# Kernel optimization log

Measured on AMD Instinct MI355X. Metric: run time of the kernel, lower is better.

The kernel has to match this reference:

```python
import jax, jax.numpy as jnp
import numpy as np

B, N, D = 1, 4096, 512
H, DH, M, WIN = 8, 64, 4, 512
QK_SCALE = 10.0  # qk_norm_scale


def _l2norm(t):
    # F.normalize(p=2, dim=-1) with groups=1
    n = jnp.linalg.norm(t, axis=-1, keepdims=True)
    return t / jnp.maximum(n, 1e-12)


def _rotate_half(t):
    t1, t2 = jnp.split(t, 2, axis=-1)
    return jnp.concatenate([-t2, t1], axis=-1)


def setup_inputs() -> dict:
    key = jax.random.key(0)
    ks = jax.random.split(key, 9)
    s = 0.02
    x = jax.random.normal(ks[0], (B, N, D), jnp.float32)
    Wq = jax.random.normal(ks[1], (D, H * DH), jnp.float32) * s
    Wk = jax.random.normal(ks[2], (D, H * DH), jnp.float32) * s
    Wv = jax.random.normal(ks[3], (D, H * DH), jnp.float32) * s
    Wg = jax.random.normal(ks[4], (D, H * DH), jnp.float32) * s
    bg = jnp.ones((H * DH,), jnp.float32)  # torch init: bias=1
    Wo = jax.random.normal(ks[5], (H * DH, D), jnp.float32) * s
    mem_k = jax.random.normal(ks[6], (H, M, DH), jnp.float32)
    mem_v = jax.random.normal(ks[7], (H, M, DH), jnp.float32)
    # standard rotary table, duplicated halves so rotate_half pairing matches
    half = DH // 2
    inv = 1.0 / (10000.0 ** (np.arange(half, dtype=np.float32) / half))
    f = np.outer(np.arange(N, dtype=np.float32), inv)  # [N, DH/2]
    freqs = jnp.asarray(np.concatenate([f, f], axis=-1), jnp.float32)  # [N, DH]
    return {"x": x, "Wq": Wq, "Wk": Wk, "Wv": Wv, "Wg": Wg, "bg": bg,
            "Wo": Wo, "mem_k": mem_k, "mem_v": mem_v, "freqs": freqs}


def reference(x, Wq, Wk, Wv, Wg, bg, Wo, mem_k, mem_v, freqs):
    # projections -> b h n d
    def split_heads(t):
        return t.reshape(B, N, H, DH).transpose(0, 2, 1, 3)
    q = split_heads(x @ Wq)
    k = split_heads(x @ Wk)
    v = split_heads(x @ Wv)
    # qk-norm (groups=1), scale handled via QK_SCALE later
    q = _l2norm(q)
    k = _l2norm(k)
    # rotary (l == DH so full head dim is rotated)
    cos = jnp.cos(freqs)  # [N, DH]
    sin = jnp.sin(freqs)
    q = q * cos + _rotate_half(q) * sin
    k = k * cos + _rotate_half(k) * sin
    # memory KV concat (mem_k goes through l2norm under qk_norm)
    mk = jnp.broadcast_to(_l2norm(mem_k)[None], (B, H, M, DH))
    mv = jnp.broadcast_to(mem_v[None], (B, H, M, DH))
    k = jnp.concatenate([mk, k], axis=2)  # [B,H,M+N,DH]
    v = jnp.concatenate([mv, v], axis=2)
    J = N + M
    # local window mask: queries at positions M..J-1, keys at 0..J-1
    rq = jnp.arange(M, J)
    rk = jnp.arange(J)
    dist = rq[:, None] - rk[None, :]
    allowed = (dist <= WIN) & (dist >= -WIN)  # [N, J]
    sim = jnp.einsum('bhid,bhjd->bhij', q, k) * QK_SCALE
    neg = -jnp.finfo(sim.dtype).max
    sim = jnp.where(allowed[None, None], sim, neg)
    attn = jax.nn.softmax(sim, axis=-1)
    out = jnp.einsum('bhij,bhjd->bhid', attn, v)  # [B,H,N,DH]
    out = out.transpose(0, 2, 1, 3).reshape(B, N, H * DH)
    # value gating
    gates = x @ Wg + bg
    out = out * jax.nn.sigmoid(gates)
    return out @ Wo
```

## Files before the change

### kernel.cpp

```cpp
#include <hip/hip_runtime.h>
#include <math.h>

#define TN 4096
#define DM 512
#define NH 8
#define DHD 64
#define MEM 4
#define WINR 512
#define JTOT (TN + MEM)
#define JPAD 4168
#define QK_SCALE 10.0f

typedef __attribute__((ext_vector_type(8))) short bf16x8;
typedef __attribute__((ext_vector_type(4))) float f32x4;

__device__ __forceinline__ unsigned short f2bf(float f) {
    unsigned u = __float_as_uint(f);
    u = (u + 0x7FFFu + ((u >> 16) & 1u)) >> 16;
    return (unsigned short)u;
}

__global__ __launch_bounds__(256)
void prep(const float* __restrict__ X, unsigned short* __restrict__ Xb,
          const float* __restrict__ W0, const float* __restrict__ W1,
          const float* __restrict__ W2, const float* __restrict__ W3,
          const float* __restrict__ W4, unsigned short* __restrict__ T,
          const float* __restrict__ freqs, float2* __restrict__ tab,
          const float* __restrict__ mem_k, const float* __restrict__ mem_v,
          unsigned short* __restrict__ k_b, unsigned short* __restrict__ v_b)
{
    const int b = blockIdx.x;
    const int t = threadIdx.x;

    if (b < 2048) {
        int idx = b * 256 + t;
        float4 v = *(const float4*)&X[(size_t)idx * 4];
        *(ushort4*)&Xb[(size_t)idx * 4] =
            make_ushort4(f2bf(v.x), f2bf(v.y), f2bf(v.z), f2bf(v.w));
    } else if (b < 2368) {
        __shared__ unsigned short Ts[64][68];
        int bi = b - 2048;
        int sel = bi >> 6, tile = bi & 63;
        const float* __restrict__ W =
            (sel == 0) ? W0 : (sel == 1) ? W1 : (sel == 2) ? W2 : (sel == 3) ? W3 : W4;
        unsigned short* __restrict__ Wt = T + (size_t)sel * DM * DM;
        int r0 = (tile >> 3) * 64, c0 = (tile & 7) * 64;
        #pragma unroll
        for (int p = 0; p < 4; ++p) {
            int i  = p * 16 + (t >> 4);
            int j4 = (t & 15) * 4;
            float4 v = *(const float4*)&W[(size_t)(r0 + i) * DM + c0 + j4];
            Ts[i][j4 + 0] = f2bf(v.x); Ts[i][j4 + 1] = f2bf(v.y);
            Ts[i][j4 + 2] = f2bf(v.z); Ts[i][j4 + 3] = f2bf(v.w);
        }
        __syncthreads();
        #pragma unroll
        for (int p = 0; p < 4; ++p) {
            int oc  = p * 16 + (t >> 4);
            int or4 = (t & 15) * 4;
            *(ushort4*)&Wt[(size_t)(c0 + oc) * DM + r0 + or4] =
                make_ushort4(Ts[or4 + 0][oc], Ts[or4 + 1][oc],
                             Ts[or4 + 2][oc], Ts[or4 + 3][oc]);
        }
    } else if (b < 2432) {
        int tid = (b - 2368) * 256 + t;
        #pragma unroll
        for (int e = 0; e < 16; ++e) {
            int id = e * 16384 + tid;
            float f = freqs[id];
            float sn, cs;
            sincosf(f, &sn, &cs);
            tab[id] = make_float2(cs, sn);
        }
    } else {
        int gw   = (b - 2432) * 4 + (t >> 6);
        int lane = t & 63;
        int h = gw >> 2, m = gw & 3;
        float kv = mem_k[(size_t)(h * MEM + m) * DHD + lane];
        float s = kv * kv;
        #pragma unroll
        for (int off = 1; off < 64; off <<= 1) s += __shfl_xor(s, off);
        kv = kv / fmaxf(sqrtf(s), 1e-12f);
        k_b[((size_t)h * JPAD + m) * 64 + lane] = f2bf(kv);
        v_b[((size_t)h * JPAD + m) * 64 + lane] =
            f2bf(mem_v[(size_t)(h * MEM + m) * DHD + lane]);
    }
}

__global__ __launch_bounds__(256)
void gemm_qkvg_mfma(const unsigned short* __restrict__ Xb,
                    const unsigned short* __restrict__ Wt,
                    const float2* __restrict__ tab,
                    const float* __restrict__ bg,
                    unsigned short* __restrict__ q_b,
                    unsigned short* __restrict__ k_b,
                    unsigned short* __restrict__ v_b,
                    float* __restrict__ graw)
{
    __shared__ __align__(16) unsigned short As[128][32];
    __shared__ __align__(16) unsigned short Bs[128][32];
    const int sel = blockIdx.z;
    const unsigned short* __restrict__ Wsel = Wt + (size_t)sel * DM * DM;
    const int row0 = blockIdx.x * 128;
    const int col0 = blockIdx.y * 128;
    const int t = threadIdx.x;
    const int w = t >> 6, l = t & 63;
    const int wm = w >> 1, wn = w & 1;
    const int l15 = l & 15, lh = l >> 4;

    f32x4 acc[4][4];
    #pragma unroll
    for (int mi = 0; mi < 4; ++mi)
        #pragma unroll
        for (int ni = 0; ni < 4; ++ni)
            acc[mi][ni] = (f32x4){0.f, 0.f, 0.f, 0.f};

    for (int k0 = 0; k0 < DM; k0 += 32) {
        __syncthreads();
        #pragma unroll
        for (int cc = 0; cc < 2; ++cc) {
            int c = t + cc * 256;
            int row = c >> 2, k8 = c & 3;
            *(bf16x8*)&As[row][k8 * 8] =
                *(const bf16x8*)&Xb[(size_t)(row0 + row) * DM + k0 + k8 * 8];
            *(bf16x8*)&Bs[row][k8 * 8] =
                *(const bf16x8*)&Wsel[(size_t)(col0 + row) * DM + k0 + k8 * 8];
        }
        __syncthreads();

        bf16x8 af[4], bfr[4];
        #pragma unroll
        for (int mi = 0; mi < 4; ++mi)
            af[mi] = *(const bf16x8*)&As[wm * 64 + mi * 16 + l15][lh * 8];
        #pragma unroll
        for (int ni = 0; ni < 4; ++ni)
            bfr[ni] = *(const bf16x8*)&Bs[wn * 64 + ni * 16 + l15][lh * 8];
        #pragma unroll
        for (int mi = 0; mi < 4; ++mi)
            #pragma unroll
            for (int ni = 0; ni < 4; ++ni)
                acc[mi][ni] = __builtin_amdgcn_mfma_f32_16x16x32_bf16(
                    af[mi], bfr[ni], acc[mi][ni], 0, 0, 0);
    }

    if (sel <= 1) {
        const int h = (col0 + wn * 64) >> 6;
        #pragma unroll
        for (int mi = 0; mi < 4; ++mi) {
            #pragma unroll
            for (int r = 0; r < 4; ++r) {
                float v0 = acc[mi][0][r], v1 = acc[mi][1][r];
                float v2 = acc[mi][2][r], v3 = acc[mi][3][r];
                float ss = v0 * v0 + v1 * v1 + v2 * v2 + v3 * v3;
                ss += __shfl_xor(ss, 1); ss += __shfl_xor(ss, 2);
                ss += __shfl_xor(ss, 4); ss += __shfl_xor(ss, 8);
                float inv = 1.0f / fmaxf(sqrtf(ss), 1e-12f);
                v0 *= inv; v1 *= inv; v2 *= inv; v3 *= inv;
                int n = row0 + wm * 64 + mi * 16 + lh * 4 + r;
                float2 t0 = tab[n * 64 + l15];
                float2 t1 = tab[n * 64 + 16 + l15];
                float o0 = v0 * t0.x - v2 * t0.y;
                float o1 = v1 * t1.x - v3 * t1.y;
                float o2 = v2 * t0.x + v0 * t0.y;
                float o3 = v3 * t1.x + v1 * t1.y;
                unsigned short* dst = (sel == 0)
                    ? &q_b[((size_t)h * TN + n) * 64]
                    : &k_b[((size_t)h * JPAD + MEM + n) * 64];
                dst[l15]      = f2bf(o0);
                dst[16 + l15] = f2bf(o1);
                dst[32 + l15] = f2bf(o2);
                dst[48 + l15] = f2bf(o3);
            }
        }
    } else if (sel == 2) {
        const int h = (col0 + wn * 64) >> 6;
        #pragma unroll
        for (int mi = 0; mi < 4; ++mi)
            #pragma unroll
            for (int ni = 0; ni < 4; ++ni) {
                int d = ni * 16 + l15;
                #pragma unroll
                for (int r = 0; r < 4; ++r) {
                    int grow = row0 + wm * 64 + mi * 16 + lh * 4 + r;
                    v_b[((size_t)h * JPAD + MEM + grow) * 64 + d] = f2bf(acc[mi][ni][r]);
                }
            }
    } else {
        #pragma unroll
        for (int mi = 0; mi < 4; ++mi)
            #pragma unroll
            for (int ni = 0; ni < 4; ++ni) {
                int gcol = col0 + wn * 64 + ni * 16 + l15;
                float bgv = bg[gcol];
                #pragma unroll
                for (int r = 0; r < 4; ++r) {
                    int grow = row0 + wm * 64 + mi * 16 + lh * 4 + r;
                    float g = acc[mi][ni][r] + bgv;
                    graw[(size_t)grow * DM + gcol] = 1.0f / (1.0f + __expf(-g));
                }
            }
    }
}

__global__ __launch_bounds__(256)
void gemm_out_mfma(const unsigned short* __restrict__ Ab,
                   const unsigned short* __restrict__ Wot,
                   float* __restrict__ C)
{
    __shared__ __align__(16) unsigned short As[128][32];
    __shared__ __align__(16) unsigned short Bs[128][32];
    const int row0 = blockIdx.x * 128;
    const int col0 = blockIdx.y * 128;
    const int t = threadIdx.x;
    const int w = t >> 6, l = t & 63;
    const int wm = w >> 1, wn = w & 1;

    f32x4 acc[4][4];
    #pragma unroll
    for (int mi = 0; mi < 4; ++mi)
        #pragma unroll
        for (int ni = 0; ni < 4; ++ni)
            acc[mi][ni] = (f32x4){0.f, 0.f, 0.f, 0.f};

    for (int k0 = 0; k0 < DM; k0 += 32) {
        __syncthreads();
        #pragma unroll
        for (int cc = 0; cc < 2; ++cc) {
            int c = t + cc * 256;
            int row = c >> 2, k8 = c & 3;
            *(bf16x8*)&As[row][k8 * 8] =
                *(const bf16x8*)&Ab[(size_t)(row0 + row) * DM + k0 + k8 * 8];
            *(bf16x8*)&Bs[row][k8 * 8] =
                *(const bf16x8*)&Wot[(size_t)(col0 + row) * DM + k0 + k8 * 8];
        }
        __syncthreads();

        bf16x8 af[4], bfr[4];
        #pragma unroll
        for (int mi = 0; mi < 4; ++mi)
            af[mi] = *(const bf16x8*)&As[wm * 64 + mi * 16 + (l & 15)][(l >> 4) * 8];
        #pragma unroll
        for (int ni = 0; ni < 4; ++ni)
            bfr[ni] = *(const bf16x8*)&Bs[wn * 64 + ni * 16 + (l & 15)][(l >> 4) * 8];
        #pragma unroll
        for (int mi = 0; mi < 4; ++mi)
            #pragma unroll
            for (int ni = 0; ni < 4; ++ni)
                acc[mi][ni] = __builtin_amdgcn_mfma_f32_16x16x32_bf16(
                    af[mi], bfr[ni], acc[mi][ni], 0, 0, 0);
    }

    #pragma unroll
    for (int mi = 0; mi < 4; ++mi)
        #pragma unroll
        for (int ni = 0; ni < 4; ++ni) {
            int gcol = col0 + wn * 64 + ni * 16 + (l & 15);
            #pragma unroll
            for (int r = 0; r < 4; ++r) {
                int grow = row0 + wm * 64 + mi * 16 + (l >> 4) * 4 + r;
                C[(size_t)grow * DM + gcol] = acc[mi][ni][r];
            }
        }
}

__global__ __launch_bounds__(256)
void attn_mfma(const unsigned short* __restrict__ qb,
               const unsigned short* __restrict__ kb,
               const unsigned short* __restrict__ vb,
               const float* __restrict__ gate,
               unsigned short* __restrict__ attnb)
{
    __shared__ __align__(16) unsigned short Qs[64][72];
    __shared__ __align__(16) unsigned short Ks[64][72];
    __shared__ __align__(16) unsigned short Vt[64][72];
    __shared__ __align__(16) unsigned short Ps[64][72];

    const int sw   = (blockIdx.x & 7) * 64 + (blockIdx.x >> 3);
    const int head = sw >> 6;
    const int n0   = (sw & 63) * 64;
    const int t = threadIdx.x;
    const int wid = t >> 6;
    const int l = t & 63;
    const int l15 = l & 15, lh = l >> 4;

    #pragma unroll
    for (int it = 0; it < 2; ++it) {
        int idx = t + it * 256;
        int row = idx >> 3, c8 = (idx & 7) * 8;
        *(bf16x8*)&Qs[row][c8] =
            *(const bf16x8*)&qb[((size_t)(head * TN + n0 + row)) * 64 + c8];
    }

    f32x4 oacc[4];
    #pragma unroll
    for (int dt = 0; dt < 4; ++dt) oacc[dt] = (f32x4){0.f, 0.f, 0.f, 0.f};
    float mrow[4] = {-3.0e38f, -3.0e38f, -3.0e38f, -3.0e38f};
    float lrow[4] = {0.f, 0.f, 0.f, 0.f};

    const int p_base = MEM + n0;
    const int kstart = max(0, p_base - WINR);
    const int kend   = min(JTOT, p_base + 63 + WINR + 1);

    const int srow = t >> 3, sc8 = (t & 7) * 8;
    const int srow2 = (t + 256) >> 3, sc82 = ((t + 256) & 7) * 8;
    const int vj = t & 63, vd0 = (t >> 6) * 8;
    const int vj2 = (t + 256) & 63, vd02 = ((t + 256) >> 6) * 8;
    bf16x8 kr0, kr1, vr0, vr1;

    kr0 = *(const bf16x8*)&kb[((size_t)head * JPAD + kstart + srow) * 64 + sc8];
    kr1 = *(const bf16x8*)&kb[((size_t)head * JPAD + kstart + srow2) * 64 + sc82];
    vr0 = *(const bf16x8*)&vb[((size_t)head * JPAD + kstart + vj) * 64 + vd0];
    vr1 = *(const bf16x8*)&vb[((size_t)head * JPAD + kstart + vj2) * 64 + vd02];

    for (int j0 = kstart; j0 < kend; j0 += 64) {
        __syncthreads();
        *(bf16x8*)&Ks[srow][sc8]   = kr0;
        *(bf16x8*)&Ks[srow2][sc82] = kr1;
        #pragma unroll
        for (int i = 0; i < 8; ++i) Vt[vd0 + i][vj]   = (unsigned short)vr0[i];
        #pragma unroll
        for (int i = 0; i < 8; ++i) Vt[vd02 + i][vj2] = (unsigned short)vr1[i];
        __syncthreads();

        if (j0 + 64 < kend) {
            int jn = j0 + 64;
            kr0 = *(const bf16x8*)&kb[((size_t)head * JPAD + jn + srow) * 64 + sc8];
            kr1 = *(const bf16x8*)&kb[((size_t)head * JPAD + jn + srow2) * 64 + sc82];
            vr0 = *(const bf16x8*)&vb[((size_t)head * JPAD + jn + vj) * 64 + vd0];
            vr1 = *(const bf16x8*)&vb[((size_t)head * JPAD + jn + vj2) * 64 + vd02];
        }

        f32x4 sacc[4];
        #pragma unroll
        for (int kt = 0; kt < 4; ++kt) sacc[kt] = (f32x4){0.f, 0.f, 0.f, 0.f};
        __builtin_amdgcn_s_setprio(1);
        #pragma unroll
        for (int s = 0; s < 2; ++s) {
            bf16x8 a = *(const bf16x8*)&Qs[wid * 16 + l15][s * 32 + lh * 8];
            #pragma unroll
            for (int kt = 0; kt < 4; ++kt) {
                bf16x8 b = *(const bf16x8*)&Ks[kt * 16 + l15][s * 32 + lh * 8];
                sacc[kt] = __builtin_amdgcn_mfma_f32_16x16x32_bf16(a, b, sacc[kt], 0, 0, 0);
            }
        }
        __builtin_amdgcn_s_setprio(0);

        #pragma unroll
        for (int r = 0; r < 4; ++r) {
            int pq = p_base + wid * 16 + lh * 4 + r;
            float sv[4];
            float tm = -3.0e38f;
            #pragma unroll
            for (int kt = 0; kt < 4; ++kt) {
                int j = j0 + kt * 16 + l15;
                int dist = pq - j;
                bool ok = (dist <= WINR) && (dist >= -WINR) && (j < JTOT);
                float val = ok ? sacc[kt][r] * QK_SCALE : -3.0e38f;
                sv[kt] = val;
                tm = fmaxf(tm, val);
            }
            #pragma unroll
            for (int off = 1; off < 16; off <<= 1) tm = fmaxf(tm, __shfl_xor(tm, off));
            float mnew = fmaxf(mrow[r], tm);
            float corr = __expf(mrow[r] - mnew);
            float rs = 0.f;
            #pragma unroll
            for (int kt = 0; kt < 4; ++kt) {
                float pe = (sv[kt] > -1.0e37f) ? __expf(sv[kt] - mnew) : 0.f;
                rs += pe;
                Ps[wid * 16 + lh * 4 + r][kt * 16 + l15] = f2bf(pe);
            }
            #pragma unroll
            for (int off = 1; off < 16; off <<= 1) rs += __shfl_xor(rs, off);
            lrow[r] = lrow[r] * corr + rs;
            mrow[r] = mnew;
            #pragma unroll
            for (int dt = 0; dt < 4; ++dt) oacc[dt][r] *= corr;
        }

        __builtin_amdgcn_s_setprio(1);
        #pragma unroll
        for (int s = 0; s < 2; ++s) {
            bf16x8 a = *(const bf16x8*)&Ps[wid * 16 + l15][s * 32 + lh * 8];
            #pragma unroll
            for (int dt = 0; dt < 4; ++dt) {
                bf16x8 b = *(const bf16x8*)&Vt[dt * 16 + l15][s * 32 + lh * 8];
                oacc[dt] = __builtin_amdgcn_mfma_f32_16x16x32_bf16(a, b, oacc[dt], 0, 0, 0);
            }
        }
        __builtin_amdgcn_s_setprio(0);
    }

    #pragma unroll
    for (int r = 0; r < 4; ++r) {
        int n = n0 + wid * 16 + lh * 4 + r;
        float inv = 1.0f / lrow[r];
        #pragma unroll
        for (int dt = 0; dt < 4; ++dt) {
            int col = head * 64 + dt * 16 + l15;
            float g = gate[(size_t)n * DM + col];
            attnb[(size_t)n * DM + col] = f2bf(oacc[dt][r] * inv * g);
        }
    }
}

extern "C" void kernel_launch(void* const* d_in, const int* in_sizes, int n_in,
                              void* d_out, int out_size, void* d_ws, size_t ws_size,
                              hipStream_t stream)
{
    const float* x     = (const float*)d_in[0];
    const float* Wq    = (const float*)d_in[1];
    const float* Wk    = (const float*)d_in[2];
    const float* Wv    = (const float*)d_in[3];
    const float* Wg    = (const float*)d_in[4];
    const float* bg    = (const float*)d_in[5];
    const float* Wo    = (const float*)d_in[6];
    const float* mem_k = (const float*)d_in[7];
    const float* mem_v = (const float*)d_in[8];
    const float* freqs = (const float*)d_in[9];

    unsigned short* q_b = (unsigned short*)d_ws;
    unsigned short* k_b = q_b + (size_t)NH * TN * DHD;
    unsigned short* v_b = k_b + (size_t)NH * JPAD * DHD;
    unsigned short* Xb  = v_b + (size_t)NH * JPAD * DHD;
    unsigned short* attnb = Xb;
    unsigned short* Wt  = Xb + (size_t)TN * DM;
    float* graw = (float*)(Wt + (size_t)5 * DM * DM);
    float2* tab = (float2*)(graw + (size_t)TN * DM);

    prep<<<dim3(2440), 256, 0, stream>>>(x, Xb, Wq, Wk, Wv, Wg, Wo, Wt,
                                         freqs, tab, mem_k, mem_v, k_b, v_b);

    gemm_qkvg_mfma<<<dim3(TN / 128, DM / 128, 4), 256, 0, stream>>>(
        Xb, Wt, tab, bg, q_b, k_b, v_b, graw);

    attn_mfma<<<dim3(512), 256, 0, stream>>>(q_b, k_b, v_b, graw, attnb);

    gemm_out_mfma<<<dim3(TN / 128, DM / 128), 256, 0, stream>>>(
        attnb, Wt + (size_t)4 * DM * DM, (float*)d_out);
}
```

Measured before the change: 173.6 us.

## Use a fixed softmax max bound from qk-norm and pad GEMM LDS tiles

Q and K are L2-normalized and rotary preserves the norm, so the scaled logits are bounded by QK_SCALE. The attention kernel therefore subtracts a constant 10 instead of tracking an online running max. This drops the per-tile max shuffles, the correction exponentials and the accumulator rescaling, and the row-sum reduction now runs once at the end. The QKVG and output GEMMs also pad their shared-memory tile rows from 32 to 40 elements to reduce LDS bank conflicts. The fixed bound is exact only because of the normalization, and it adds a small risk of underflow for logits near the lower bound.

```diff
diff --git a/kernel.cpp b/kernel.cpp
--- a/kernel.cpp
+++ b/kernel.cpp
@@ -10,6 +10,7 @@
 #define JTOT (TN + MEM)
 #define JPAD 4168
 #define QK_SCALE 10.0f
+#define LDA 40
 
 typedef __attribute__((ext_vector_type(8))) short bf16x8;
 typedef __attribute__((ext_vector_type(4))) float f32x4;
@@ -97,8 +98,8 @@
                     unsigned short* __restrict__ v_b,
                     float* __restrict__ graw)
 {
-    __shared__ __align__(16) unsigned short As[128][32];
-    __shared__ __align__(16) unsigned short Bs[128][32];
+    __shared__ __align__(16) unsigned short As[128][LDA];
+    __shared__ __align__(16) unsigned short Bs[128][LDA];
     const int sel = blockIdx.z;
     const unsigned short* __restrict__ Wsel = Wt + (size_t)sel * DM * DM;
     const int row0 = blockIdx.x * 128;
@@ -207,8 +208,8 @@
                    const unsigned short* __restrict__ Wot,
                    float* __restrict__ C)
 {
-    __shared__ __align__(16) unsigned short As[128][32];
-    __shared__ __align__(16) unsigned short Bs[128][32];
+    __shared__ __align__(16) unsigned short As[128][LDA];
+    __shared__ __align__(16) unsigned short Bs[128][LDA];
     const int row0 = blockIdx.x * 128;
     const int col0 = blockIdx.y * 128;
     const int t = threadIdx.x;
@@ -294,8 +295,7 @@
     f32x4 oacc[4];
     #pragma unroll
     for (int dt = 0; dt < 4; ++dt) oacc[dt] = (f32x4){0.f, 0.f, 0.f, 0.f};
-    float mrow[4] = {-3.0e38f, -3.0e38f, -3.0e38f, -3.0e38f};
-    float lrow[4] = {0.f, 0.f, 0.f, 0.f};
+    float lpart[4] = {0.f, 0.f, 0.f, 0.f};
 
     const int p_base = MEM + n0;
     const int kstart = max(0, p_base - WINR);
@@ -348,34 +348,15 @@
         #pragma unroll
         for (int r = 0; r < 4; ++r) {
             int pq = p_base + wid * 16 + lh * 4 + r;
-            float sv[4];
-            float tm = -3.0e38f;
             #pragma unroll
             for (int kt = 0; kt < 4; ++kt) {
                 int j = j0 + kt * 16 + l15;
                 int dist = pq - j;
                 bool ok = (dist <= WINR) && (dist >= -WINR) && (j < JTOT);
-                float val = ok ? sacc[kt][r] * QK_SCALE : -3.0e38f;
-                sv[kt] = val;
-                tm = fmaxf(tm, val);
-            }
-            #pragma unroll
-            for (int off = 1; off < 16; off <<= 1) tm = fmaxf(tm, __shfl_xor(tm, off));
-            float mnew = fmaxf(mrow[r], tm);
-            float corr = __expf(mrow[r] - mnew);
-            float rs = 0.f;
-            #pragma unroll
-            for (int kt = 0; kt < 4; ++kt) {
-                float pe = (sv[kt] > -1.0e37f) ? __expf(sv[kt] - mnew) : 0.f;
-                rs += pe;
+                float pe = ok ? __expf(sacc[kt][r] * QK_SCALE - 10.0f) : 0.f;
+                lpart[r] += pe;
                 Ps[wid * 16 + lh * 4 + r][kt * 16 + l15] = f2bf(pe);
             }
-            #pragma unroll
-            for (int off = 1; off < 16; off <<= 1) rs += __shfl_xor(rs, off);
-            lrow[r] = lrow[r] * corr + rs;
-            mrow[r] = mnew;
-            #pragma unroll
-            for (int dt = 0; dt < 4; ++dt) oacc[dt][r] *= corr;
         }
 
         __builtin_amdgcn_s_setprio(1);
@@ -393,8 +374,11 @@
 
     #pragma unroll
     for (int r = 0; r < 4; ++r) {
+        float rs = lpart[r];
+        rs += __shfl_xor(rs, 1); rs += __shfl_xor(rs, 2);
+        rs += __shfl_xor(rs, 4); rs += __shfl_xor(rs, 8);
+        float inv = 1.0f / rs;
         int n = n0 + wid * 16 + lh * 4 + r;
-        float inv = 1.0f / lrow[r];
         #pragma unroll
         for (int dt = 0; dt < 4; ++dt) {
             int col = head * 64 + dt * 16 + l15;
```

Result: faster. 159.8 us (-7.9%).
